# Kernel tuning notes

Hardware: AMD Instinct MI355X
Metric: run time of the kernel (lower is better)

The kernel has to match this reference:

```python
import jax, jax.numpy as jnp
import numpy as np

KERNEL_SIZE = 5
SIGMA_SPACE = 1.0
SIGMA_COLOR = 0.1
PAD = KERNEL_SIZE // 2


def make_spatial_kernel(kernel_size, sigma_space):
    r = kernel_size // 2
    coords = jnp.arange(-r, r + 1, dtype=jnp.float32)
    xx, yy = jnp.meshgrid(coords, coords, indexing='ij')
    return jnp.exp(-(xx ** 2 + yy ** 2) / (2.0 * sigma_space ** 2))  # [K, K]


def setup_inputs() -> dict:
    key = jax.random.key(0)
    x = jax.random.uniform(key, (4, 3, 512, 512), dtype=jnp.float32)
    spatial_kernel = make_spatial_kernel(KERNEL_SIZE, SIGMA_SPACE)
    sigma_color = jnp.float32(SIGMA_COLOR)
    return {"x": x, "spatial_kernel": spatial_kernel, "sigma_color": sigma_color}


def reference(x, spatial_kernel, sigma_color):
    # x: [B, C, H, W]; spatial_kernel: [K, K] (fixed buffer, computed at init)
    B, C, H, W = x.shape
    K = KERNEL_SIZE
    padded = jnp.pad(x, ((0, 0), (0, 0), (PAD, PAD), (PAD, PAD)), mode='reflect')
    # Gather KxK windows as a trailing tap axis: [B, C, H, W, K*K]
    patches = jnp.stack(
        [padded[:, :, i:i + H, j:j + W] for i in range(K) for j in range(K)],
        axis=-1,
    )
    sk = spatial_kernel.reshape(-1)  # [K*K]
    color_diff = patches - x[..., None]
    color_weight = jnp.exp(-(color_diff ** 2) / (2.0 * sigma_color ** 2))
    weight = sk * color_weight  # [B, C, H, W, K*K]
    weight = weight / (jnp.sum(weight, axis=-1, keepdims=True) + 1e-8)
    return jnp.sum(weight * patches, axis=-1)  # [B, C, H, W]
```

## Files before the change

### kernel.cpp

```cpp
#include <hip/hip_runtime.h>

typedef float v2f __attribute__((ext_vector_type(2)));

constexpr int H = 512, W = 512;
constexpr int K = 5, PADR = 2;

__device__ __forceinline__ float rfl(float v) {
    union { float f; int i; } u; u.f = v;
    u.i = __builtin_amdgcn_readfirstlane(u.i);
    return u.f;
}

constexpr int idx6(int d2) {
    return d2 == 0 ? 0 : d2 == 1 ? 1 : d2 == 2 ? 2 : d2 == 4 ? 3 : d2 == 5 ? 4 : 5;
}

__global__ __launch_bounds__(256) void bilateral_kernel(
    const float* __restrict__ x,
    const float* __restrict__ sk,
    const float* __restrict__ sigma_color,
    float* __restrict__ out)
{
    int t = threadIdx.x;

    float lw[6];
    lw[0] = rfl(__builtin_amdgcn_logf(sk[12]));
    lw[1] = rfl(__builtin_amdgcn_logf(sk[7]));
    lw[2] = rfl(__builtin_amdgcn_logf(sk[6]));
    lw[3] = rfl(__builtin_amdgcn_logf(sk[2]));
    lw[4] = rfl(__builtin_amdgcn_logf(sk[1]));
    lw[5] = rfl(__builtin_amdgcn_logf(sk[0]));

    float s = sigma_color[0];
    float c2 = -1.4426950408889634f / (2.0f * s * s);
    v2f c2v = { c2, c2 };

    int gid = blockIdx.x * 256 + t;
    int p0 = gid << 3;
    int w0 = p0 & (W - 1);
    int row = p0 >> 9;
    int h = row & (H - 1);
    int plane = row >> 9;
    const float* xp = x + (size_t)plane * (H * W);

    bool lane0 = (w0 == 0);
    bool laneN = (w0 == W - 8);
    int wL = lane0 ? 0        : (w0 - 4);
    int wR = laneN ? (w0 + 4) : (w0 + 8);

    v2f cc[4], ws[4], acc[4];
#pragma unroll
    for (int q = 0; q < 4; ++q) { ws[q] = (v2f){0.f, 0.f}; acc[q] = (v2f){0.f, 0.f}; }

    constexpr int order[K] = {2, 0, 1, 3, 4};
#pragma unroll
    for (int oi = 0; oi < K; ++oi) {
        const int i = order[oi];
        int hv = h + i - PADR;
        hv = (hv < 0) ? -hv : hv;
        hv = (hv >= H) ? (2 * H - 2 - hv) : hv;
        const float* rp = xp + (hv << 9);

        float4 a  = *(const float4*)(rp + wL);
        float4 m0 = *(const float4*)(rp + w0);
        float4 m1 = *(const float4*)(rp + w0 + 4);
        float4 b  = *(const float4*)(rp + wR);

        float win[12];
        win[0]  = lane0 ? m0.z : a.z;
        win[1]  = lane0 ? m0.y : a.w;
        win[2]  = m0.x; win[3] = m0.y; win[4] = m0.z; win[5] = m0.w;
        win[6]  = m1.x; win[7] = m1.y; win[8] = m1.z; win[9] = m1.w;
        win[10] = laneN ? m1.z : b.x;
        win[11] = laneN ? m1.y : b.y;

        if (oi == 0) {
#pragma unroll
            for (int q = 0; q < 4; ++q) {
                cc[q][0] = win[2 * q + 2];
                cc[q][1] = win[2 * q + 3];
            }
        }

#pragma unroll
        for (int j = 0; j < K; ++j) {
            const float lwv = lw[idx6((i - 2) * (i - 2) + (j - 2) * (j - 2))];
            v2f lsp = { lwv, lwv };
#pragma unroll
            for (int q = 0; q < 4; ++q) {
                v2f v = { win[2 * q + j], win[2 * q + j + 1] };
                v2f d = v - cc[q];
                v2f arg = __builtin_elementwise_fma(d * c2v, d, lsp);
                v2f wq;
                wq[0] = __builtin_amdgcn_exp2f(arg[0]);
                wq[1] = __builtin_amdgcn_exp2f(arg[1]);
                ws[q] += wq;
                acc[q] = __builtin_elementwise_fma(wq, v, acc[q]);
            }
        }
    }

    float4 o0, o1;
    o0.x = acc[0][0] * __builtin_amdgcn_rcpf(ws[0][0] + 1e-8f);
    o0.y = acc[0][1] * __builtin_amdgcn_rcpf(ws[0][1] + 1e-8f);
    o0.z = acc[1][0] * __builtin_amdgcn_rcpf(ws[1][0] + 1e-8f);
    o0.w = acc[1][1] * __builtin_amdgcn_rcpf(ws[1][1] + 1e-8f);
    o1.x = acc[2][0] * __builtin_amdgcn_rcpf(ws[2][0] + 1e-8f);
    o1.y = acc[2][1] * __builtin_amdgcn_rcpf(ws[2][1] + 1e-8f);
    o1.z = acc[3][0] * __builtin_amdgcn_rcpf(ws[3][0] + 1e-8f);
    o1.w = acc[3][1] * __builtin_amdgcn_rcpf(ws[3][1] + 1e-8f);
    *(float4*)(out + p0)     = o0;
    *(float4*)(out + p0 + 4) = o1;
}

extern "C" void kernel_launch(void* const* d_in, const int* in_sizes, int n_in,
                              void* d_out, int out_size, void* d_ws, size_t ws_size,
                              hipStream_t stream) {
    const float* x  = (const float*)d_in[0];
    const float* sk = (const float*)d_in[1];
    const float* sc = (const float*)d_in[2];
    float* out = (float*)d_out;

    const int total = in_sizes[0];
    const int blocks = total / (256 * 8);
    bilateral_kernel<<<blocks, 256, 0, stream>>>(x, sk, sc, out);
}
```

Baseline: 79.28 us.

## Stage row tile plus halo in LDS and read stencil taps from shared memory

```diff
diff --git a/kernel.cpp b/kernel.cpp
--- a/kernel.cpp
+++ b/kernel.cpp
@@ -4,6 +4,8 @@
 
 constexpr int H = 512, W = 512;
 constexpr int K = 5, PADR = 2;
+constexpr int ROWS = 4;
+constexpr int SROWS = ROWS + 4;
 
 __device__ __forceinline__ float rfl(float v) {
     union { float f; int i; } u; u.f = v;
@@ -15,13 +17,17 @@
     return d2 == 0 ? 0 : d2 == 1 ? 1 : d2 == 2 ? 2 : d2 == 4 ? 3 : d2 == 5 ? 4 : 5;
 }
 
-__global__ __launch_bounds__(256) void bilateral_kernel(
+__global__ __launch_bounds__(256, 4) void bilateral_kernel(
     const float* __restrict__ x,
     const float* __restrict__ sk,
     const float* __restrict__ sigma_color,
     float* __restrict__ out)
 {
+    __shared__ float lds[SROWS][W];
+
     int t = threadIdx.x;
+    int wave = t >> 6;
+    int l = t & 63;
 
     float lw[6];
     lw[0] = rfl(__builtin_amdgcn_logf(sk[12]));
@@ -35,17 +41,30 @@
     float c2 = -1.4426950408889634f / (2.0f * s * s);
     v2f c2v = { c2, c2 };
 
-    int gid = blockIdx.x * 256 + t;
-    int p0 = gid << 3;
-    int w0 = p0 & (W - 1);
-    int row = p0 >> 9;
-    int h = row & (H - 1);
-    int plane = row >> 9;
+    int plane = blockIdx.x >> 7;
+    int r0 = (blockIdx.x & 127) * ROWS;
     const float* xp = x + (size_t)plane * (H * W);
 
-    bool lane0 = (w0 == 0);
-    bool laneN = (w0 == W - 8);
-    int wL = lane0 ? 0        : (w0 - 4);
+#pragma unroll
+    for (int kk = 0; kk < 2; ++kk) {
+        int k = wave + 4 * kk;
+        int gr = r0 - 2 + k;
+        gr = (gr < 0) ? -gr : gr;
+        gr = (gr >= H) ? (2 * H - 2 - gr) : gr;
+        const float* src = xp + (gr << 9) + (l << 3);
+        float4 v0 = *(const float4*)(src);
+        float4 v1 = *(const float4*)(src + 4);
+        *(float4*)(&lds[k][l << 3])     = v0;
+        *(float4*)(&lds[k][(l << 3) + 4]) = v1;
+    }
+    __syncthreads();
+
+    int rr = wave;
+    int w0 = l << 3;
+
+    bool lane0 = (l == 0);
+    bool laneN = (l == 63);
+    int wL = lane0 ? 0       : (w0 - 4);
     int wR = laneN ? (w0 + 4) : (w0 + 8);
 
     v2f cc[4], ws[4], acc[4];
@@ -56,10 +75,7 @@
 #pragma unroll
     for (int oi = 0; oi < K; ++oi) {
         const int i = order[oi];
-        int hv = h + i - PADR;
-        hv = (hv < 0) ? -hv : hv;
-        hv = (hv >= H) ? (2 * H - 2 - hv) : hv;
-        const float* rp = xp + (hv << 9);
+        const float* rp = &lds[rr + i][0];
 
         float4 a  = *(const float4*)(rp + wL);
         float4 m0 = *(const float4*)(rp + w0);
@@ -100,6 +116,7 @@
         }
     }
 
+    float* op = out + (size_t)plane * (H * W) + ((r0 + rr) << 9) + w0;
     float4 o0, o1;
     o0.x = acc[0][0] * __builtin_amdgcn_rcpf(ws[0][0] + 1e-8f);
     o0.y = acc[0][1] * __builtin_amdgcn_rcpf(ws[0][1] + 1e-8f);
@@ -109,8 +126,8 @@
     o1.y = acc[2][1] * __builtin_amdgcn_rcpf(ws[2][1] + 1e-8f);
     o1.z = acc[3][0] * __builtin_amdgcn_rcpf(ws[3][0] + 1e-8f);
     o1.w = acc[3][1] * __builtin_amdgcn_rcpf(ws[3][1] + 1e-8f);
-    *(float4*)(out + p0)     = o0;
-    *(float4*)(out + p0 + 4) = o1;
+    *(float4*)(op)     = o0;
+    *(float4*)(op + 4) = o1;
 }
 
 extern "C" void kernel_launch(void* const* d_in, const int* in_sizes, int n_in,
```

New measurement: 78.48 us. About the same (-1.0%).
